# Kernel optimization log

Measured on AMD Instinct MI355X. Metric: run time of the kernel, lower is better.

The kernel has to match this reference:

```python
import jax, jax.numpy as jnp
import numpy as np
from jax import lax

B, CIN, COUT, H, W = 8, 256, 256, 96, 96


def _conv_bn(x, w, g, b, act):
    # 3x3 conv, stride 1, SAME padding (NCHW / OIHW), then per-channel affine (folded BN)
    y = lax.conv_general_dilated(x, w, (1, 1), 'SAME',
                                 dimension_numbers=('NCHW', 'OIHW', 'NCHW'))
    y = y * g[None, :, None, None] + b[None, :, None, None]
    return jax.nn.relu(y) if act else y


def setup_inputs() -> dict:
    key = jax.random.key(0)
    ks = jax.random.split(key, 16)
    def wgt(k, cout, cin):
        return jax.random.normal(k, (cout, cin, 3, 3), jnp.float32) * (1.0 / np.sqrt(cin * 9))
    def gb(k, c):
        k1, k2 = jax.random.split(k)
        return (1.0 + 0.1 * jax.random.normal(k1, (c,), jnp.float32),
                0.1 * jax.random.normal(k2, (c,), jnp.float32))
    g_p1, b_p1 = gb(ks[1], COUT); g_p2, b_p2 = gb(ks[3], COUT)
    g_p, b_p = gb(ks[5], COUT); g_c1, b_c1 = gb(ks[7], COUT); g_c2, b_c2 = gb(ks[9], COUT)
    return {
        'x': jax.random.normal(ks[0], (B, CIN, H, W), jnp.float32),
        'w_p1': wgt(ks[10], COUT, CIN), 'g_p1': g_p1, 'b_p1': b_p1,
        'w_p2': wgt(ks[11], COUT, CIN), 'g_p2': g_p2, 'b_p2': b_p2,
        'w_p': wgt(ks[12], COUT, COUT), 'g_p': g_p, 'b_p': b_p,
        'w_c1': wgt(ks[13], COUT, CIN), 'g_c1': g_c1, 'b_c1': b_c1,
        'w_c2': wgt(ks[14], COUT, COUT), 'g_c2': g_c2, 'b_c2': b_c2,
    }


def reference(x, w_p1, g_p1, b_p1, w_p2, g_p2, b_p2, w_p, g_p, b_p,
              w_c1, g_c1, b_c1, w_c2, g_c2, b_c2):
    # branch 1: conv -> TopPool (cummax up, i.e. reverse along H) -> BottomPool (cummax down)
    p1 = _conv_bn(x, w_p1, g_p1, b_p1, act=True)
    pool1 = lax.cummax(p1, axis=2, reverse=True)   # TopPool
    pool1 = lax.cummax(pool1, axis=2)              # BottomPool
    # branch 2: conv -> LeftPool (reverse along W) -> RightPool
    p2 = _conv_bn(x, w_p2, g_p2, b_p2, act=True)
    pool2 = lax.cummax(p2, axis=3, reverse=True)   # LeftPool
    pool2 = lax.cummax(pool2, axis=3)              # RightPool
    p_conv = _conv_bn(pool1 + pool2, w_p, g_p, b_p, act=False)
    conv1 = _conv_bn(x, w_c1, g_c1, b_c1, act=False)
    relu = jax.nn.relu(p_conv + conv1)
    return _conv_bn(relu, w_c2, g_c2, b_c2, act=True)
```

## Files before the change

### kernel.cpp

```cpp
#include <hip/hip_runtime.h>


typedef _Float16 f16x8 __attribute__((ext_vector_type(8)));
typedef _Float16 f16x4v __attribute__((ext_vector_type(4)));
typedef float f32x4 __attribute__((ext_vector_type(4)));

#define HP 98
#define WP 98
#define KTOT 2304
#define WSET (256*KTOT)
#define XPAD_E ((size_t)8*HP*WP*256)
#define UVP_E  ((size_t)8*98*256)
#define UV2_E  ((size_t)3*8*96*256)
#define WUV_SET 196608

#define BUF_B 12288
#define SMEM_B 24576

struct Ctx {
  unsigned goff[3];
  unsigned lds_stage;
  unsigned aoff;
  int wl, quad, wv;
  int b, h0, w0;
};

template<int TR>
__device__ __forceinline__ Ctx make_ctx(int spatial)
{
  Ctx c;
  c.b = spatial / 72;
  const int tt = spatial - c.b * 72;
  if (TR == 0) { const int ht = tt / 6,  wt = tt - ht * 6;  c.h0 = ht * 8;  c.w0 = wt * 16; }
  else         { const int ht = tt / 12, wt = tt - ht * 12; c.h0 = ht * 16; c.w0 = wt * 8;  }
  const int tid = threadIdx.x, lane = tid & 63;
  c.wv = tid >> 6;
  c.quad = lane >> 4; c.wl = lane & 15;
  c.aoff = (unsigned)(c.wv * 4 * 512 + c.wl * 32 + c.quad * 8);
  const unsigned base_hw = (unsigned)(c.b * HP + c.h0) * WP + c.w0;
#pragma unroll
  for (int t = 0; t < 3; ++t) {
    int pos = (c.wv * 3 + t) * 16 + (lane >> 2);
    if (pos > 179) pos = 179;
    const int wh = (TR == 0) ? pos / 18 : pos / 10;
    const int ww = (TR == 0) ? pos - wh * 18 : pos - wh * 10;
    c.goff[t] = (base_hw + (unsigned)(wh * WP + ww)) * 256u + (lane & 3) * 8u;
  }
  c.lds_stage = (unsigned)(c.wv * 3) * 1024u + (unsigned)lane * 16u;
  return c;
}

__device__ __forceinline__ void stage_cb(const _Float16* __restrict__ src,
                                         char* sbuf, const Ctx& c, int buf, int cb)
{
  char* l0 = sbuf + buf * BUF_B + c.lds_stage;
#pragma unroll
  for (int t = 0; t < 3; ++t) {
    const _Float16* g = src + c.goff[t] + cb * 32;
    __builtin_amdgcn_global_load_lds(
        (const __attribute__((address_space(1))) void*)g,
        (__attribute__((address_space(3))) void*)(l0 + t * 1024), 16, 0, 0);
  }
}

template<int TR>
__device__ __forceinline__ void conv_accum(const _Float16* __restrict__ src,
                                           const _Float16* __restrict__ wkb,
                                           char* sbuf, const Ctx& c, f32x4 acc[4][8])
{
  const _Float16* A0 = wkb + c.aoff;
  stage_cb(src, sbuf, c, 0, 0);
#pragma unroll 1
  for (int cb = 0; cb < 8; ++cb) {
    __syncthreads();
    if (cb < 7) stage_cb(src, sbuf, c, (cb + 1) & 1, cb + 1);
    const _Float16* B = (const _Float16*)(sbuf + (cb & 1) * BUF_B);
    const _Float16* A = A0 + cb * (9 * 8192);
#pragma unroll
    for (int o = 0; o < 3; ++o) {
      f16x8 cache[10];
#pragma unroll
      for (int r = 0; r < 10; ++r)
        cache[r] = (TR == 0)
            ? *(const f16x8*)(B + (r * 18 + c.wl + o) * 32 + c.quad * 8)
            : *(const f16x8*)(B + ((c.wl + o) * 10 + r) * 32 + c.quad * 8);
#pragma unroll
      for (int p = 0; p < 3; ++p) {
        const int tap = (TR == 0) ? p * 3 + o : o * 3 + p;
        f16x8 af[4];
#pragma unroll
        for (int i = 0; i < 4; ++i)
          af[i] = *(const f16x8*)(A + tap * 8192 + i * 512);
#pragma unroll
        for (int i = 0; i < 4; ++i)
#pragma unroll
          for (int j = 0; j < 8; ++j)
            acc[i][j] = __builtin_amdgcn_mfma_f32_16x16x32_f16(af[i], cache[j + p], acc[i][j], 0, 0, 0);
      }
    }
  }
  __syncthreads();
}

#define ZERO_ACC8(acc) \
  _Pragma("unroll") for (int i = 0; i < 4; ++i) \
  _Pragma("unroll") for (int j = 0; j < 8; ++j) acc[i][j] = (f32x4){0.f,0.f,0.f,0.f};

#define BUF_BS 24576
#define SMEM_BS 49152

struct CtxS {
  unsigned goff[6];
  unsigned lds_stage;
  unsigned aoff;
  int hl, wl, quad;
  int co_wg;
  int b, h0, w0;
};

__device__ __forceinline__ CtxS make_ctxS(int spatial, int co_wg)
{
  CtxS c;
  c.co_wg = co_wg;
  c.b = spatial / 36;
  const int tt = spatial - c.b * 36;
  const int ht = tt / 6, wt = tt - ht * 6;
  c.h0 = ht * 16; c.w0 = wt * 16;
  const int tid = threadIdx.x, lane = tid & 63, wv = tid >> 6;
  c.quad = lane >> 4; c.wl = lane & 15;
  c.hl = wv * 4;
  c.aoff = (unsigned)(c.wl * 32 + c.quad * 8);
  const unsigned base_hw = (unsigned)(c.b * HP + c.h0) * WP + c.w0;
#pragma unroll
  for (int t = 0; t < 6; ++t) {
    int pos = (wv * 6 + t) * 16 + (lane >> 2);
    if (pos > 323) pos = 323;
    const int wh = pos / 18, ww = pos - wh * 18;
    c.goff[t] = (base_hw + (unsigned)(wh * WP + ww)) * 256u + (lane & 3) * 8u;
  }
  c.lds_stage = (unsigned)(wv * 6) * 1024u + (unsigned)lane * 16u;
  return c;
}

__device__ __forceinline__ void stage_cbS(const _Float16* __restrict__ src,
                                          char* sbuf, const CtxS& c, int buf, int cb)
{
  char* l0 = sbuf + buf * BUF_BS + c.lds_stage;
#pragma unroll
  for (int t = 0; t < 6; ++t) {
    const _Float16* g = src + c.goff[t] + cb * 32;
    __builtin_amdgcn_global_load_lds(
        (const __attribute__((address_space(1))) void*)g,
        (__attribute__((address_space(3))) void*)(l0 + t * 1024), 16, 0, 0);
  }
}

__device__ __forceinline__ void conv_accumS(const _Float16* __restrict__ src,
                                            const _Float16* __restrict__ wkb,
                                            char* sbuf, const CtxS& c,
                                            f32x4 acc[4][4])
{
  const _Float16* A0 = wkb + c.aoff;
  const int rbase = (c.hl * 18 + c.wl) * 32 + c.quad * 8;
  stage_cbS(src, sbuf, c, 0, 0);
#pragma unroll 1
  for (int cb = 0; cb < 8; ++cb) {
    __syncthreads();
    if (cb < 7) stage_cbS(src, sbuf, c, (cb + 1) & 1, cb + 1);
    const _Float16* B = (const _Float16*)(sbuf + (cb & 1) * BUF_BS);
    const _Float16* A = A0 + cb * (9 * 8192);
#pragma unroll
    for (int dw = 0; dw < 3; ++dw) {
      f16x8 row[6];
#pragma unroll
      for (int r = 0; r < 6; ++r)
        row[r] = *(const f16x8*)(B + rbase + (r * 18 + dw) * 32);
#pragma unroll
      for (int dh = 0; dh < 3; ++dh) {
        f16x8 af[4];
#pragma unroll
        for (int i = 0; i < 4; ++i)
          af[i] = *(const f16x8*)(A + (dh * 3 + dw) * 8192 + i * 512);
#pragma unroll
        for (int i = 0; i < 4; ++i)
#pragma unroll
          for (int j = 0; j < 4; ++j)
            acc[i][j] = __builtin_amdgcn_mfma_f32_16x16x32_f16(af[i], row[j + dh], acc[i][j], 0, 0, 0);
      }
    }
  }
  __syncthreads();
}

__global__ __launch_bounds__(256, 2) void k_conv_p12(
    const _Float16* __restrict__ xpad, const _Float16* __restrict__ wk,
    const float* __restrict__ bias1, const float* __restrict__ bias2,
    float* __restrict__ u_pad, float* __restrict__ v_pad)
{
  __shared__ __align__(16) char smem[SMEM_B];
  const int lin = blockIdx.x;
  const int set = lin >= 576;
  const int spatial = lin - set * 576;
  f32x4 acc[4][8];
  ZERO_ACC8(acc)
  if (set == 0) {
    Ctx c = make_ctx<0>(spatial);
    conv_accum<0>(xpad, wk, smem, c, acc);
#pragma unroll
    for (int i = 0; i < 4; ++i) {
      const int co = c.wv * 64 + i * 16 + c.quad * 4;
      const float4 bs = *(const float4*)(bias1 + co);
      float m0 = 0.f, m1 = 0.f, m2 = 0.f, m3 = 0.f;
#pragma unroll
      for (int j = 0; j < 8; ++j) {
        m0 = fmaxf(m0, acc[i][j][0] + bs.x);
        m1 = fmaxf(m1, acc[i][j][1] + bs.y);
        m2 = fmaxf(m2, acc[i][j][2] + bs.z);
        m3 = fmaxf(m3, acc[i][j][3] + bs.w);
      }
      unsigned* tgt = (unsigned*)(u_pad + ((size_t)c.b * 98 + (c.w0 + c.wl + 1)) * 256 + co);
      atomicMax(tgt + 0, __float_as_uint(m0));
      atomicMax(tgt + 1, __float_as_uint(m1));
      atomicMax(tgt + 2, __float_as_uint(m2));
      atomicMax(tgt + 3, __float_as_uint(m3));
    }
  } else {
    Ctx c = make_ctx<1>(spatial);
    conv_accum<1>(xpad, wk + WSET, smem, c, acc);
#pragma unroll
    for (int i = 0; i < 4; ++i) {
      const int co = c.wv * 64 + i * 16 + c.quad * 4;
      const float4 bs = *(const float4*)(bias2 + co);
      float m0 = 0.f, m1 = 0.f, m2 = 0.f, m3 = 0.f;
#pragma unroll
      for (int j = 0; j < 8; ++j) {
        m0 = fmaxf(m0, acc[i][j][0] + bs.x);
        m1 = fmaxf(m1, acc[i][j][1] + bs.y);
        m2 = fmaxf(m2, acc[i][j][2] + bs.z);
        m3 = fmaxf(m3, acc[i][j][3] + bs.w);
      }
      unsigned* tgt = (unsigned*)(v_pad + ((size_t)c.b * 98 + (c.h0 + c.wl + 1)) * 256 + co);
      atomicMax(tgt + 0, __float_as_uint(m0));
      atomicMax(tgt + 1, __float_as_uint(m1));
      atomicMax(tgt + 2, __float_as_uint(m2));
      atomicMax(tgt + 3, __float_as_uint(m3));
    }
  }
}

__global__ __launch_bounds__(256, 2) void k_uv1d(
    const float* __restrict__ u_pad, const float* __restrict__ v_pad,
    const _Float16* __restrict__ wuv, float* __restrict__ u2, float* __restrict__ v2)
{
  const int id = blockIdx.x;
  const int b = id & 7, cs = (id >> 3) % 3, t = id / 24;
  const float* src = t ? v_pad : u_pad;
  float* dst = t ? v2 : u2;
  const _Float16* A0 = wuv + (size_t)(t * 3 + cs) * WUV_SET;
  const int lane = threadIdx.x & 63, wv = threadIdx.x >> 6;
  const int quad = lane >> 4, l16 = lane & 15;

  f32x4 acc[4][6];
#pragma unroll
  for (int i = 0; i < 4; ++i)
#pragma unroll
    for (int j = 0; j < 6; ++j) acc[i][j] = (f32x4){0.f, 0.f, 0.f, 0.f};

#pragma unroll 1
  for (int kb = 0; kb < 24; ++kb) {
    const int dw = kb >> 3, cb = kb & 7;
    f16x8 bf[6];
#pragma unroll
    for (int j = 0; j < 6; ++j) {
      const int pos = j * 16 + l16;
      const float* p = src + ((size_t)b * 98 + (pos + dw)) * 256 + cb * 32 + quad * 8;
      const float4 x0 = *(const float4*)p;
      const float4 x1 = *(const float4*)(p + 4);
      f16x8 v;
      v[0] = (_Float16)x0.x; v[1] = (_Float16)x0.y; v[2] = (_Float16)x0.z; v[3] = (_Float16)x0.w;
      v[4] = (_Float16)x1.x; v[5] = (_Float16)x1.y; v[6] = (_Float16)x1.z; v[7] = (_Float16)x1.w;
      bf[j] = v;
    }
    f16x8 af[4];
#pragma unroll
    for (int i = 0; i < 4; ++i)
      af[i] = *(const f16x8*)(A0 + (size_t)(kb * 16 + wv * 4 + i) * 512 + l16 * 32 + quad * 8);
#pragma unroll
    for (int i = 0; i < 4; ++i)
#pragma unroll
      for (int j = 0; j < 6; ++j)
        acc[i][j] = __builtin_amdgcn_mfma_f32_16x16x32_f16(af[i], bf[j], acc[i][j], 0, 0, 0);
  }
#pragma unroll
  for (int i = 0; i < 4; ++i)
#pragma unroll
    for (int j = 0; j < 6; ++j) {
      const int pos = j * 16 + l16;
      const int co = wv * 64 + i * 16 + quad * 4;
      *(f32x4*)(dst + ((size_t)(cs * 8 + b) * 96 + pos) * 256 + co) = acc[i][j];
    }
}

__global__ __launch_bounds__(256, 3) void k_conv_c1f(
    const _Float16* __restrict__ xpad, const _Float16* __restrict__ wkc1,
    const float* __restrict__ bias_p, const float* __restrict__ bias_c1,
    const float* __restrict__ u2, const float* __restrict__ v2,
    _Float16* __restrict__ rpad)
{
  __shared__ __align__(16) char smem[SMEM_BS];
  const int lin = blockIdx.x;
  const int co_blk = lin / 288, spatial = lin - co_blk * 288;
  CtxS c = make_ctxS(spatial, co_blk * 64);
  f32x4 acc[4][4];
#pragma unroll
  for (int i = 0; i < 4; ++i)
#pragma unroll
    for (int j = 0; j < 4; ++j) acc[i][j] = (f32x4){0.f, 0.f, 0.f, 0.f};
  conv_accumS(xpad, wkc1 + co_blk * (4 * 512), smem, c, acc);

  const int w = c.w0 + c.wl;
  const int wcase = (w == 0) ? 0 : ((w == 95) ? 2 : 1);
  _Float16* lt = (_Float16*)smem;
#pragma unroll
  for (int fa = 0; fa < 4; ++fa) {
    const int co_l = fa * 16 + c.quad * 4;
    float4 bs = *(const float4*)(bias_p + c.co_wg + co_l);
    const float4 b2 = *(const float4*)(bias_c1 + c.co_wg + co_l);
    bs.x += b2.x; bs.y += b2.y; bs.z += b2.z; bs.w += b2.w;
#pragma unroll
    for (int fb = 0; fb < 4; ++fb) {
      const int h = c.h0 + c.hl + fb;
      const int hcase = (h == 0) ? 0 : ((h == 95) ? 2 : 1);
      const float4 uq = *(const float4*)(u2 + ((size_t)(hcase * 8 + c.b) * 96 + w) * 256 + c.co_wg + co_l);
      const float4 vq = *(const float4*)(v2 + ((size_t)(wcase * 8 + c.b) * 96 + h) * 256 + c.co_wg + co_l);
      const int n_l = (c.hl + fb) * 16 + c.wl;
      f16x4v pk;
      pk[0] = (_Float16)fmaxf(acc[fa][fb][0] + bs.x + uq.x + vq.x, 0.f);
      pk[1] = (_Float16)fmaxf(acc[fa][fb][1] + bs.y + uq.y + vq.y, 0.f);
      pk[2] = (_Float16)fmaxf(acc[fa][fb][2] + bs.z + uq.z + vq.z, 0.f);
      pk[3] = (_Float16)fmaxf(acc[fa][fb][3] + bs.w + uq.w + vq.w, 0.f);
      *(f16x4v*)&lt[n_l * 68 + co_l] = pk;
    }
  }
  __syncthreads();
  _Float16* out_base = rpad + ((size_t)(c.b * HP + c.h0 + 1) * WP + c.w0 + 1) * 256;
  const int cc = threadIdx.x & 7, rr = threadIdx.x >> 3;
#pragma unroll
  for (int pass = 0; pass < 8; ++pass) {
    const int n_l = pass * 32 + rr;
    const int hh = n_l >> 4, ww = n_l & 15;
    uint2 q0 = *(const uint2*)&lt[n_l * 68 + cc * 8];
    uint2 q1 = *(const uint2*)&lt[n_l * 68 + cc * 8 + 4];
    *(uint4*)(out_base + (size_t)hh * (WP * 256) + ww * 256 + c.co_wg + cc * 8) =
        make_uint4(q0.x, q0.y, q1.x, q1.y);
  }
}

__global__ __launch_bounds__(256, 3) void k_conv_c2(
    const _Float16* __restrict__ rpad, const _Float16* __restrict__ wkc2,
    const float* __restrict__ bias, float* __restrict__ dout)
{
  __shared__ __align__(16) char smem[SMEM_BS];
  const int lin = blockIdx.x;
  const int co_blk = lin / 288, spatial = lin - co_blk * 288;
  CtxS c = make_ctxS(spatial, co_blk * 64);
  f32x4 acc[4][4];
#pragma unroll
  for (int i = 0; i < 4; ++i)
#pragma unroll
    for (int j = 0; j < 4; ++j) acc[i][j] = (f32x4){0.f, 0.f, 0.f, 0.f};
  conv_accumS(rpad, wkc2 + co_blk * (4 * 512), smem, c, acc);
#pragma unroll
  for (int fb = 0; fb < 4; ++fb) {
    const int h = c.h0 + c.hl + fb;
    const int w = c.w0 + c.wl;
    float* op = dout + (size_t)c.b * 2359296 + h * 96 + w;
#pragma unroll
    for (int fa = 0; fa < 4; ++fa) {
      const int co = c.co_wg + fa * 16 + c.quad * 4;
      const float4 bs = *(const float4*)(bias + co);
      op[(size_t)(co + 0) * 9216] = fmaxf(acc[fa][fb][0] + bs.x, 0.f);
      op[(size_t)(co + 1) * 9216] = fmaxf(acc[fa][fb][1] + bs.y, 0.f);
      op[(size_t)(co + 2) * 9216] = fmaxf(acc[fa][fb][2] + bs.z, 0.f);
      op[(size_t)(co + 3) * 9216] = fmaxf(acc[fa][fb][3] + bs.w, 0.f);
    }
  }
}

__global__ void k_border(_Float16* __restrict__ xpad, _Float16* __restrict__ rpad)
{
  const int idx = blockIdx.x, b = blockIdx.y;
  _Float16* buf = blockIdx.z ? rpad : xpad;
  int h, w;
  if (idx < 98)       { h = 0;  w = idx; }
  else if (idx < 196) { h = 97; w = idx - 98; }
  else { const int r = idx - 196; h = 1 + (r >> 1); w = (r & 1) ? 97 : 0; }
  buf[((size_t)(b * HP + h) * WP + w) * 256 + threadIdx.x] = (_Float16)0.f;
}

__global__ void k_pack_x(const float* __restrict__ x, _Float16* __restrict__ xpad)
{
  __shared__ float tile[32][33];
  const int bh = blockIdx.x;
  const int b = bh / 96, h = bh - b * 96;
  const int c0 = blockIdx.y * 32, w0 = blockIdx.z * 32;
  const int tx = threadIdx.x & 31, ty = threadIdx.x >> 5;
#pragma unroll
  for (int i = 0; i < 4; ++i) {
    int cI = c0 + ty + i * 8;
    tile[ty + i * 8][tx] = x[(((size_t)b * 256 + cI) * 96 + h) * 96 + w0 + tx];
  }
  __syncthreads();
#pragma unroll
  for (int i = 0; i < 4; ++i) {
    int w = w0 + ty + i * 8;
    xpad[((size_t)(b * HP + h + 1) * WP + (w + 1)) * 256 + c0 + tx] =
        (_Float16)tile[tx][ty + i * 8];
  }
}

__global__ void k_repack_w(const float* w0, const float* g0, const float* w1, const float* g1,
                           const float* w2, const float* g2, const float* w3, const float* g3,
                           const float* w4, const float* g4, _Float16* __restrict__ wk)
{
  const int set = blockIdx.y;
  const float* w; const float* g;
  switch (set) {
    case 0: w = w0; g = g0; break;
    case 1: w = w1; g = g1; break;
    case 2: w = w2; g = g2; break;
    case 3: w = w3; g = g3; break;
    default: w = w4; g = g4; break;
  }
  const int t = blockIdx.x * 256 + threadIdx.x;
  const int co = t >> 8, ci = t & 255;
  const int cb = ci >> 5, kk = ci & 31, cog = co >> 4, m = co & 15;
  const float gv = g[co];
  const float* src = w + ((size_t)co * 256 + ci) * 9;
  _Float16* dst = wk + (size_t)set * WSET + cog * 512 + m * 32 + kk;
#pragma unroll
  for (int tap = 0; tap < 9; ++tap)
    dst[(cb * 9 + tap) * 8192] = (_Float16)(src[tap] * gv);
}

__global__ void k_repack_uvw(const float* __restrict__ wp, const float* __restrict__ gp,
                             _Float16* __restrict__ wuv)
{
  const int tcs = blockIdx.y;
  const int tt = tcs / 3, cs = tcs - tt * 3;
  const int idx = blockIdx.x * 256 + threadIdx.x;
  const int co = idx >> 8, ci = idx & 255;
  const float gv = gp[co];
  const float* src = wp + ((size_t)co * 256 + ci) * 9;
  const int lo = (cs == 0) ? 1 : 0, hi = (cs == 2) ? 1 : 2;
  _Float16* base = wuv + (size_t)tcs * WUV_SET;
#pragma unroll
  for (int d = 0; d < 3; ++d) {
    float s = 0.f;
    for (int e = lo; e <= hi; ++e)
      s += (tt == 0) ? src[e * 3 + d] : src[d * 3 + e];
    const int k = d * 256 + ci;
    const int kb = k >> 5, kk = k & 31;
    base[(size_t)(kb * 16 + (co >> 4)) * 512 + (co & 15) * 32 + kk] = (_Float16)(s * gv);
  }
}

extern "C" void kernel_launch(void* const* d_in, const int* in_sizes, int n_in,
                              void* d_out, int out_size, void* d_ws, size_t ws_size,
                              hipStream_t stream)
{
  const float* x    = (const float*)d_in[0];
  const float* w_p1 = (const float*)d_in[1];
  const float* g_p1 = (const float*)d_in[2];
  const float* b_p1 = (const float*)d_in[3];
  const float* w_p2 = (const float*)d_in[4];
  const float* g_p2 = (const float*)d_in[5];
  const float* b_p2 = (const float*)d_in[6];
  const float* w_p  = (const float*)d_in[7];
  const float* g_p  = (const float*)d_in[8];
  const float* b_p  = (const float*)d_in[9];
  const float* w_c1 = (const float*)d_in[10];
  const float* g_c1 = (const float*)d_in[11];
  const float* b_c1 = (const float*)d_in[12];
  const float* w_c2 = (const float*)d_in[13];
  const float* g_c2 = (const float*)d_in[14];
  const float* b_c2 = (const float*)d_in[15];

  char* ws = (char*)d_ws;
  size_t off = 0;
  _Float16* x_pad = (_Float16*)(ws + off); off += XPAD_E * 2;
  _Float16* r_pad = (_Float16*)(ws + off); off += XPAD_E * 2;
  _Float16* wks   = (_Float16*)(ws + off); off += (size_t)5 * WSET * 2;
  _Float16* wuv   = (_Float16*)(ws + off); off += (size_t)6 * WUV_SET * 2;
  float*    u_pad = (float*)(ws + off);    off += UVP_E * 4;
  float*    v_pad = (float*)(ws + off);    off += UVP_E * 4;
  float*    u2    = (float*)(ws + off);    off += UV2_E * 4;
  float*    v2    = (float*)(ws + off);    off += UV2_E * 4;
  (void)ws_size; (void)in_sizes; (void)n_in; (void)out_size;

  hipMemsetAsync(u_pad, 0, UVP_E * 4, stream);
  hipMemsetAsync(v_pad, 0, UVP_E * 4, stream);

  k_border    <<<dim3(388, 8, 2), 256, 0, stream>>>(x_pad, r_pad);
  k_pack_x    <<<dim3(768, 8, 3), 256, 0, stream>>>(x, x_pad);
  k_repack_w  <<<dim3(256, 5),    256, 0, stream>>>(w_p1, g_p1, w_p2, g_p2, w_p, g_p,
                                                    w_c1, g_c1, w_c2, g_c2, wks);
  k_repack_uvw<<<dim3(256, 6),    256, 0, stream>>>(w_p, g_p, wuv);
  k_conv_p12  <<<1152, 256, 0, stream>>>(x_pad, wks, b_p1, b_p2, u_pad, v_pad);
  k_uv1d      <<<48,   256, 0, stream>>>(u_pad, v_pad, wuv, u2, v2);
  k_conv_c1f  <<<1152, 256, 0, stream>>>(x_pad, wks + (size_t)3 * WSET, b_p, b_c1,
                                         u2, v2, r_pad);
  k_conv_c2   <<<1152, 256, 0, stream>>>(r_pad, wks + (size_t)4 * WSET, b_c2,
                                         (float*)d_out);
}
```

Before: 640.6 us.

## Retile c1/c2 convs to full-Cout 4x16 spatial tiles and add XCD swizzle

The c1 and c2 convolutions move from 16x16 spatial tiles with a 64-channel Cout split per workgroup to 4x16 spatial tiles where each workgroup covers all 256 output channels (64 per wave). The input halo per workgroup shrinks and LDS use drops, so input staging is not repeated across four Cout blocks. The c1 epilogue now writes rpad straight from registers instead of transposing through LDS. A block-index swizzle spreads neighbouring blocks across XCDs to improve L2 locality. The trade-offs are a higher halo-to-tile ratio and less coalesced epilogue stores.

```diff
diff --git a/kernel.cpp b/kernel.cpp
--- a/kernel.cpp
+++ b/kernel.cpp
@@ -13,6 +13,11 @@
 #define UVP_E  ((size_t)8*98*256)
 #define UV2_E  ((size_t)3*8*96*256)
 #define WUV_SET 196608
+
+__device__ __forceinline__ int xcd_swz(int bid, int nwg)
+{
+  return (bid & 7) * (nwg >> 3) + (bid >> 3);
+}
 
 #define BUF_B 12288
 #define SMEM_B 24576
@@ -106,86 +111,94 @@
   _Pragma("unroll") for (int i = 0; i < 4; ++i) \
   _Pragma("unroll") for (int j = 0; j < 8; ++j) acc[i][j] = (f32x4){0.f,0.f,0.f,0.f};
 
-#define BUF_BS 24576
-#define SMEM_BS 49152
-
-struct CtxS {
-  unsigned goff[6];
+#define BUF_W 7168
+#define SMEM_W 14336
+
+struct Ctx4 {
+  unsigned goff[2];
   unsigned lds_stage;
   unsigned aoff;
-  int hl, wl, quad;
-  int co_wg;
+  int nrow;
+  int wl, quad, wv;
   int b, h0, w0;
 };
 
-__device__ __forceinline__ CtxS make_ctxS(int spatial, int co_wg)
-{
-  CtxS c;
-  c.co_wg = co_wg;
-  c.b = spatial / 36;
-  const int tt = spatial - c.b * 36;
-  const int ht = tt / 6, wt = tt - ht * 6;
-  c.h0 = ht * 16; c.w0 = wt * 16;
-  const int tid = threadIdx.x, lane = tid & 63, wv = tid >> 6;
+template<int TR>
+__device__ __forceinline__ Ctx4 make_ctx4(int spatial)
+{
+  Ctx4 c;
+  c.b = spatial / 144;
+  const int tt = spatial - c.b * 144;
+  if (TR == 0) { const int ht = tt / 6,  wt = tt - ht * 6;  c.h0 = ht * 4;  c.w0 = wt * 16; }
+  else         { const int ht = tt / 24, wt = tt - ht * 24; c.h0 = ht * 16; c.w0 = wt * 4;  }
+  const int tid = threadIdx.x, lane = tid & 63;
+  c.wv = tid >> 6;
   c.quad = lane >> 4; c.wl = lane & 15;
-  c.hl = wv * 4;
-  c.aoff = (unsigned)(c.wl * 32 + c.quad * 8);
+  c.aoff = (unsigned)(c.wv * 4 * 512 + c.wl * 32 + c.quad * 8);
   const unsigned base_hw = (unsigned)(c.b * HP + c.h0) * WP + c.w0;
-#pragma unroll
-  for (int t = 0; t < 6; ++t) {
-    int pos = (wv * 6 + t) * 16 + (lane >> 2);
-    if (pos > 323) pos = 323;
-    const int wh = pos / 18, ww = pos - wh * 18;
+  const int r0 = c.wv * 2;
+  c.nrow = (c.wv < 3) ? 2 : 1;
+#pragma unroll
+  for (int t = 0; t < 2; ++t) {
+    int row = r0 + t; if (row > 6) row = 6;
+    int pos = row * 16 + (lane >> 2);
+    if (pos > 107) pos = 107;
+    const int wh = (TR == 0) ? pos / 18 : pos / 6;
+    const int ww = (TR == 0) ? pos - wh * 18 : pos - wh * 6;
     c.goff[t] = (base_hw + (unsigned)(wh * WP + ww)) * 256u + (lane & 3) * 8u;
   }
-  c.lds_stage = (unsigned)(wv * 6) * 1024u + (unsigned)lane * 16u;
+  c.lds_stage = (unsigned)r0 * 1024u + (unsigned)lane * 16u;
   return c;
 }
 
-__device__ __forceinline__ void stage_cbS(const _Float16* __restrict__ src,
-                                          char* sbuf, const CtxS& c, int buf, int cb)
-{
-  char* l0 = sbuf + buf * BUF_BS + c.lds_stage;
-#pragma unroll
-  for (int t = 0; t < 6; ++t) {
-    const _Float16* g = src + c.goff[t] + cb * 32;
-    __builtin_amdgcn_global_load_lds(
-        (const __attribute__((address_space(1))) void*)g,
-        (__attribute__((address_space(3))) void*)(l0 + t * 1024), 16, 0, 0);
-  }
-}
-
-__device__ __forceinline__ void conv_accumS(const _Float16* __restrict__ src,
+__device__ __forceinline__ void stage_cb4(const _Float16* __restrict__ src,
+                                          char* sbuf, const Ctx4& c, int buf, int cb)
+{
+  char* l0 = sbuf + buf * BUF_W + c.lds_stage;
+#pragma unroll
+  for (int t = 0; t < 2; ++t) {
+    if (t < c.nrow) {
+      const _Float16* g = src + c.goff[t] + cb * 32;
+      __builtin_amdgcn_global_load_lds(
+          (const __attribute__((address_space(1))) void*)g,
+          (__attribute__((address_space(3))) void*)(l0 + t * 1024), 16, 0, 0);
+    }
+  }
+}
+
+template<int TR>
+__device__ __forceinline__ void conv_accum4(const _Float16* __restrict__ src,
                                             const _Float16* __restrict__ wkb,
-                                            char* sbuf, const CtxS& c,
-                                            f32x4 acc[4][4])
+                                            char* sbuf, const Ctx4& c, f32x4 acc[4][4])
 {
   const _Float16* A0 = wkb + c.aoff;
-  const int rbase = (c.hl * 18 + c.wl) * 32 + c.quad * 8;
-  stage_cbS(src, sbuf, c, 0, 0);
+  stage_cb4(src, sbuf, c, 0, 0);
 #pragma unroll 1
   for (int cb = 0; cb < 8; ++cb) {
     __syncthreads();
-    if (cb < 7) stage_cbS(src, sbuf, c, (cb + 1) & 1, cb + 1);
-    const _Float16* B = (const _Float16*)(sbuf + (cb & 1) * BUF_BS);
+    if (cb < 7) stage_cb4(src, sbuf, c, (cb + 1) & 1, cb + 1);
+    const _Float16* B = (const _Float16*)(sbuf + (cb & 1) * BUF_W);
     const _Float16* A = A0 + cb * (9 * 8192);
 #pragma unroll
-    for (int dw = 0; dw < 3; ++dw) {
-      f16x8 row[6];
+    for (int o = 0; o < 3; ++o) {
+      f16x8 cache[6];
 #pragma unroll
       for (int r = 0; r < 6; ++r)
-        row[r] = *(const f16x8*)(B + rbase + (r * 18 + dw) * 32);
-#pragma unroll
-      for (int dh = 0; dh < 3; ++dh) {
+        cache[r] = (TR == 0)
+            ? *(const f16x8*)(B + (r * 18 + c.wl + o) * 32 + c.quad * 8)
+            : *(const f16x8*)(B + ((c.wl + o) * 6 + r) * 32 + c.quad * 8);
+#pragma unroll
+      for (int p = 0; p < 3; ++p) {
+        const int tap = (TR == 0) ? p * 3 + o : o * 3 + p;
         f16x8 af[4];
 #pragma unroll
         for (int i = 0; i < 4; ++i)
-          af[i] = *(const f16x8*)(A + (dh * 3 + dw) * 8192 + i * 512);
+          af[i] = *(const f16x8*)(A + tap * 8192 + i * 512);
 #pragma unroll
         for (int i = 0; i < 4; ++i)
 #pragma unroll
           for (int j = 0; j < 4; ++j)
-            acc[i][j] = __builtin_amdgcn_mfma_f32_16x16x32_f16(af[i], row[j + dh], acc[i][j], 0, 0, 0);
+            acc[i][j] = __builtin_amdgcn_mfma_f32_16x16x32_f16(af[i], cache[j + p], acc[i][j], 0, 0, 0);
       }
     }
   }
@@ -198,7 +211,7 @@
     float* __restrict__ u_pad, float* __restrict__ v_pad)
 {
   __shared__ __align__(16) char smem[SMEM_B];
-  const int lin = blockIdx.x;
+  const int lin = xcd_swz(blockIdx.x, 1152);
   const int set = lin >= 576;
   const int spatial = lin - set * 576;
   f32x4 acc[4][8];
@@ -307,52 +320,37 @@
     const float* __restrict__ u2, const float* __restrict__ v2,
     _Float16* __restrict__ rpad)
 {
-  __shared__ __align__(16) char smem[SMEM_BS];
-  const int lin = blockIdx.x;
-  const int co_blk = lin / 288, spatial = lin - co_blk * 288;
-  CtxS c = make_ctxS(spatial, co_blk * 64);
+  __shared__ __align__(16) char smem[SMEM_W];
+  const int lin = xcd_swz(blockIdx.x, 1152);
+  Ctx4 c = make_ctx4<0>(lin);
   f32x4 acc[4][4];
 #pragma unroll
   for (int i = 0; i < 4; ++i)
 #pragma unroll
     for (int j = 0; j < 4; ++j) acc[i][j] = (f32x4){0.f, 0.f, 0.f, 0.f};
-  conv_accumS(xpad, wkc1 + co_blk * (4 * 512), smem, c, acc);
+  conv_accum4<0>(xpad, wkc1, smem, c, acc);
 
   const int w = c.w0 + c.wl;
   const int wcase = (w == 0) ? 0 : ((w == 95) ? 2 : 1);
-  _Float16* lt = (_Float16*)smem;
-#pragma unroll
-  for (int fa = 0; fa < 4; ++fa) {
-    const int co_l = fa * 16 + c.quad * 4;
-    float4 bs = *(const float4*)(bias_p + c.co_wg + co_l);
-    const float4 b2 = *(const float4*)(bias_c1 + c.co_wg + co_l);
+#pragma unroll
+  for (int i = 0; i < 4; ++i) {
+    const int co = c.wv * 64 + i * 16 + c.quad * 4;
+    float4 bs = *(const float4*)(bias_p + co);
+    const float4 b2 = *(const float4*)(bias_c1 + co);
     bs.x += b2.x; bs.y += b2.y; bs.z += b2.z; bs.w += b2.w;
 #pragma unroll
-    for (int fb = 0; fb < 4; ++fb) {
-      const int h = c.h0 + c.hl + fb;
+    for (int j = 0; j < 4; ++j) {
+      const int h = c.h0 + j;
       const int hcase = (h == 0) ? 0 : ((h == 95) ? 2 : 1);
-      const float4 uq = *(const float4*)(u2 + ((size_t)(hcase * 8 + c.b) * 96 + w) * 256 + c.co_wg + co_l);
-      const float4 vq = *(const float4*)(v2 + ((size_t)(wcase * 8 + c.b) * 96 + h) * 256 + c.co_wg + co_l);
-      const int n_l = (c.hl + fb) * 16 + c.wl;
+      const float4 uq = *(const float4*)(u2 + ((size_t)(hcase * 8 + c.b) * 96 + w) * 256 + co);
+      const float4 vq = *(const float4*)(v2 + ((size_t)(wcase * 8 + c.b) * 96 + h) * 256 + co);
       f16x4v pk;
-      pk[0] = (_Float16)fmaxf(acc[fa][fb][0] + bs.x + uq.x + vq.x, 0.f);
-      pk[1] = (_Float16)fmaxf(acc[fa][fb][1] + bs.y + uq.y + vq.y, 0.f);
-      pk[2] = (_Float16)fmaxf(acc[fa][fb][2] + bs.z + uq.z + vq.z, 0.f);
-      pk[3] = (_Float16)fmaxf(acc[fa][fb][3] + bs.w + uq.w + vq.w, 0.f);
-      *(f16x4v*)&lt[n_l * 68 + co_l] = pk;
-    }
-  }
-  __syncthreads();
-  _Float16* out_base = rpad + ((size_t)(c.b * HP + c.h0 + 1) * WP + c.w0 + 1) * 256;
-  const int cc = threadIdx.x & 7, rr = threadIdx.x >> 3;
-#pragma unroll
-  for (int pass = 0; pass < 8; ++pass) {
-    const int n_l = pass * 32 + rr;
-    const int hh = n_l >> 4, ww = n_l & 15;
-    uint2 q0 = *(const uint2*)&lt[n_l * 68 + cc * 8];
-    uint2 q1 = *(const uint2*)&lt[n_l * 68 + cc * 8 + 4];
-    *(uint4*)(out_base + (size_t)hh * (WP * 256) + ww * 256 + c.co_wg + cc * 8) =
-        make_uint4(q0.x, q0.y, q1.x, q1.y);
+      pk[0] = (_Float16)fmaxf(acc[i][j][0] + bs.x + uq.x + vq.x, 0.f);
+      pk[1] = (_Float16)fmaxf(acc[i][j][1] + bs.y + uq.y + vq.y, 0.f);
+      pk[2] = (_Float16)fmaxf(acc[i][j][2] + bs.z + uq.z + vq.z, 0.f);
+      pk[3] = (_Float16)fmaxf(acc[i][j][3] + bs.w + uq.w + vq.w, 0.f);
+      *(f16x4v*)(rpad + ((size_t)(c.b * HP + h + 1) * WP + w + 1) * 256 + co) = pk;
+    }
   }
 }
 
@@ -360,29 +358,29 @@
     const _Float16* __restrict__ rpad, const _Float16* __restrict__ wkc2,
     const float* __restrict__ bias, float* __restrict__ dout)
 {
-  __shared__ __align__(16) char smem[SMEM_BS];
-  const int lin = blockIdx.x;
-  const int co_blk = lin / 288, spatial = lin - co_blk * 288;
-  CtxS c = make_ctxS(spatial, co_blk * 64);
+  __shared__ __align__(16) char smem[SMEM_W];
+  const int lin = xcd_swz(blockIdx.x, 1152);
+  Ctx4 c = make_ctx4<0>(lin);
   f32x4 acc[4][4];
 #pragma unroll
   for (int i = 0; i < 4; ++i)
 #pragma unroll
     for (int j = 0; j < 4; ++j) acc[i][j] = (f32x4){0.f, 0.f, 0.f, 0.f};
-  conv_accumS(rpad, wkc2 + co_blk * (4 * 512), smem, c, acc);
-#pragma unroll
-  for (int fb = 0; fb < 4; ++fb) {
-    const int h = c.h0 + c.hl + fb;
-    const int w = c.w0 + c.wl;
+  conv_accum4<0>(rpad, wkc2, smem, c, acc);
+
+  const int w = c.w0 + c.wl;
+#pragma unroll
+  for (int j = 0; j < 4; ++j) {
+    const int h = c.h0 + j;
     float* op = dout + (size_t)c.b * 2359296 + h * 96 + w;
 #pragma unroll
-    for (int fa = 0; fa < 4; ++fa) {
-      const int co = c.co_wg + fa * 16 + c.quad * 4;
+    for (int i = 0; i < 4; ++i) {
+      const int co = c.wv * 64 + i * 16 + c.quad * 4;
       const float4 bs = *(const float4*)(bias + co);
-      op[(size_t)(co + 0) * 9216] = fmaxf(acc[fa][fb][0] + bs.x, 0.f);
-      op[(size_t)(co + 1) * 9216] = fmaxf(acc[fa][fb][1] + bs.y, 0.f);
-      op[(size_t)(co + 2) * 9216] = fmaxf(acc[fa][fb][2] + bs.z, 0.f);
-      op[(size_t)(co + 3) * 9216] = fmaxf(acc[fa][fb][3] + bs.w, 0.f);
+      op[(size_t)(co + 0) * 9216] = fmaxf(acc[i][j][0] + bs.x, 0.f);
+      op[(size_t)(co + 1) * 9216] = fmaxf(acc[i][j][1] + bs.y, 0.f);
+      op[(size_t)(co + 2) * 9216] = fmaxf(acc[i][j][2] + bs.z, 0.f);
+      op[(size_t)(co + 3) * 9216] = fmaxf(acc[i][j][3] + bs.w, 0.f);
     }
   }
 }
```

Result: faster. 602.5 us (-6.0%).
